# Optimization experiments

Measured on AMD Instinct MI355X. Metric: run time of the kernel, lower is better.

The kernel has to match this reference:

```python
import jax, jax.numpy as jnp
import numpy as np

D_MODEL = 4096
EXPERTS = 64
TOPK = 2


def setup_inputs() -> dict:
    key = jax.random.key(0)
    kx, kw = jax.random.split(key)
    x = jax.random.normal(kx, (4, 4096, D_MODEL), dtype=jnp.float32)
    # nn.Linear(input_size, expert_num, bias=False) weight, stored as [D, E] for x @ W
    W = jax.random.normal(kw, (D_MODEL, EXPERTS), dtype=jnp.float32) * (1.0 / np.sqrt(D_MODEL))
    return {"x": x, "W": W}


def reference(x, W):
    # logits = GateL(x): [B, S, E]
    logits = jnp.einsum("bsd,de->bse", x, W)
    y = jax.nn.softmax(logits, axis=-1)
    # top-k mask: scatter ones at top-k expert slots, zero elsewhere
    _, topk_idx = jax.lax.top_k(y, TOPK)            # [B, S, k]
    mask = jnp.sum(jax.nn.one_hot(topk_idx, EXPERTS, dtype=y.dtype), axis=-2)  # [B, S, E]
    y = y * mask
    return (y, logits)
```

## Files before the change

kernel.cpp:

```cpp
#include <hip/hip_runtime.h>
#include <hip/hip_bf16.h>


typedef float f32x4 __attribute__((ext_vector_type(4)));
typedef __bf16 bf16x8 __attribute__((ext_vector_type(8)));

#define MFMA16(a, b, c) __builtin_amdgcn_mfma_f32_16x16x32_bf16((a), (b), (c), 0, 0, 0)

__device__ __forceinline__ void gload_lds16(const void* g, void* l) {
  __builtin_amdgcn_global_load_lds((const __attribute__((address_space(1))) void*)g,
                                   (__attribute__((address_space(3))) void*)l, 16, 0, 0);
}

__global__ __launch_bounds__(256) void k_prep_w(const float* __restrict__ W,
                                                __bf16* __restrict__ wsW) {
  const int c = blockIdx.x;
  const int t = threadIdx.x;
  const int e = t & 63;
  const int q = t >> 6;
  const int nh = e >> 5, ntl = (e >> 4) & 1, ln = e & 15;
  bf16x8 hi8, lo8;
#pragma unroll
  for (int j = 0; j < 8; ++j) {
    const float w = W[(size_t)(c * 32 + q * 8 + j) * 64 + e];
    const __bf16 h = (__bf16)w;
    hi8[j] = h;
    lo8[j] = (__bf16)(w - (float)h);
  }
  __bf16* base = wsW + (size_t)c * 4096 + nh * 2048 + ntl * 1024 + q * 128 + ln * 8;
  *(bf16x8*)base = hi8;
  *(bf16x8*)(base + 512) = lo8;
}

__device__ __forceinline__ void split8(const f32x4 a, const f32x4 b,
                                       bf16x8& hi, bf16x8& lo) {
  const float f[8] = {a.x, a.y, a.z, a.w, b.x, b.y, b.z, b.w};
#pragma unroll
  for (int i = 0; i < 8; ++i) {
    const unsigned u = __builtin_bit_cast(unsigned, f[i]);
    hi[i] = __builtin_bit_cast(__bf16, (unsigned short)(u >> 16));
    lo[i] = (__bf16)(f[i] - __builtin_bit_cast(float, u & 0xFFFF0000u));
  }
}

__global__ __launch_bounds__(256, 2) void k_gate(const float* __restrict__ x,
                                                 const __bf16* __restrict__ wsW,
                                                 float* __restrict__ y,
                                                 float* __restrict__ logits) {
  __shared__ __align__(16) char smem[57344];
  const int t = threadIdx.x, w = t >> 6, l = t & 63;
  const int tb = blockIdx.x * 32;
  const int mt = w & 1, nh = w >> 1;
  const int q = l >> 4, ln = l & 15;

  char* xw = smem + w * 6144;
  char* ww = smem + 24576 + w * 8192;

  const int r0 = l >> 3, g0 = (l & 7) ^ (r0 & 7);
  const int r1 = 8 + (l >> 3), g1 = (l & 7) ^ (r1 & 7);
  const float* xp0 = x + (size_t)(tb + mt * 16 + r0) * 4096 + g0 * 4;
  const float* xp1 = x + (size_t)(tb + mt * 16 + r1) * 4096 + g1 * 4;
  const __bf16* wg = wsW + nh * 2048 + l * 8;

  const int rA = ln;
  const int offA0 = (rA * 8 + ((2 * q) ^ (rA & 7))) * 16;
  const int offA1 = (rA * 8 + ((2 * q + 1) ^ (rA & 7))) * 16;
  const int offW = q * 256 + ln * 16;

  auto stageX = [&](int st, int c) {
    char* d = xw + st * 2048 + l * 16;
    gload_lds16(xp0 + (size_t)c * 32, d);
    gload_lds16(xp1 + (size_t)c * 32, d + 1024);
  };
  auto stageW = [&](int st, int c) {
    char* d = ww + st * 4096 + l * 16;
    const __bf16* s = wg + (size_t)c * 4096;
    gload_lds16(s, d);
    gload_lds16(s + 512, d + 1024);
    gload_lds16(s + 1024, d + 2048);
    gload_lds16(s + 1536, d + 3072);
  };

  f32x4 acc0 = {0.f, 0.f, 0.f, 0.f};
  f32x4 acc1 = {0.f, 0.f, 0.f, 0.f};

  stageX(0, 0); stageW(0, 0); stageX(1, 1); stageW(1, 1); stageX(2, 2);

  int st = 0, stw = 0;
  for (int c = 0; c < 128; ++c) {
    if (c < 126)       asm volatile("s_waitcnt vmcnt(8)" ::: "memory");
    else if (c == 126) asm volatile("s_waitcnt vmcnt(6)" ::: "memory");
    else               asm volatile("s_waitcnt vmcnt(0)" ::: "memory");

    const char* xb = xw + st * 2048;
    const char* wb = ww + stw * 4096;
    const f32x4 A = *(const f32x4*)(xb + offA0);
    const f32x4 B = *(const f32x4*)(xb + offA1);
    const bf16x8 wh0 = *(const bf16x8*)(wb + offW);
    const bf16x8 wl0 = *(const bf16x8*)(wb + offW + 1024);
    const bf16x8 wh1 = *(const bf16x8*)(wb + offW + 2048);
    const bf16x8 wl1 = *(const bf16x8*)(wb + offW + 3072);

    bf16x8 ah, al;
    split8(A, B, ah, al);
    acc0 = MFMA16(ah, wh0, acc0);
    acc0 = MFMA16(al, wh0, acc0);
    acc0 = MFMA16(ah, wl0, acc0);
    acc0 = MFMA16(al, wl0, acc0);
    acc1 = MFMA16(ah, wh1, acc1);
    acc1 = MFMA16(al, wh1, acc1);
    acc1 = MFMA16(ah, wl1, acc1);
    acc1 = MFMA16(al, wl1, acc1);

    if (c < 126) stageW(stw, c + 2);
    if (c < 125) stageX(st, c + 3);
    st = (st == 2) ? 0 : st + 1;
    stw ^= 1;
  }

  __syncthreads();
  float* lt = (float*)smem;
  const int col = nh * 32 + ln;
#pragma unroll
  for (int r = 0; r < 4; ++r) {
    const int row = mt * 16 + q * 4 + r;
    lt[row * 65 + col] = acc0[r];
    lt[row * 65 + col + 16] = acc1[r];
    logits[(size_t)(tb + row) * 64 + col] = acc0[r];
    logits[(size_t)(tb + row) * 64 + col + 16] = acc1[r];
  }
  __syncthreads();

#pragma unroll
  for (int i = 0; i < 8; ++i) {
    const int tok = w * 8 + i;
    const float v = lt[tok * 65 + l];
    float bv = v; int bi = l;
    for (int off = 32; off; off >>= 1) {
      const float ov = __shfl_xor(bv, off);
      const int oi = __shfl_xor(bi, off);
      if (ov > bv || (ov == bv && oi < bi)) { bv = ov; bi = oi; }
    }
    const int i1 = bi;
    const float m1 = bv;
    float cv = (l == i1) ? -3.402823466e38f : v;
    int ci = l;
    for (int off = 32; off; off >>= 1) {
      const float ov = __shfl_xor(cv, off);
      const int oi = __shfl_xor(ci, off);
      if (ov > cv || (ov == cv && oi < ci)) { cv = ov; ci = oi; }
    }
    const float e = __expf(v - m1);
    float s = e;
    for (int off = 32; off; off >>= 1) s += __shfl_xor(s, off);
    y[(size_t)(tb + tok) * 64 + l] = (l == i1 || l == ci) ? (e / s) : 0.0f;
  }
}

extern "C" void kernel_launch(void* const* d_in, const int* in_sizes, int n_in,
                              void* d_out, int out_size, void* d_ws, size_t ws_size,
                              hipStream_t stream) {
  (void)in_sizes; (void)n_in; (void)out_size; (void)ws_size;
  const float* x = (const float*)d_in[0];
  const float* W = (const float*)d_in[1];
  float* out = (float*)d_out;
  float* yout = out;
  float* logits = out + 1048576;
  __bf16* wsW = (__bf16*)d_ws;

  k_prep_w<<<128, 256, 0, stream>>>(W, wsW);
  k_gate<<<512, 256, 0, stream>>>(x, wsW, yout, logits);
}
```

Before: 415.7 us.

## Shrink gate tile to 16 tokens with shared x buffer and register W prefetch

Each block now handles 16 tokens instead of 32, and the grid doubles to 1024 blocks. The four waves split the 64 experts between them and share one double-buffered LDS tile of x instead of each wave staging its own x and W. W fragments are prefetched directly into registers from global memory one chunk ahead, and a __syncthreads per iteration replaces the manual vmcnt pipeline. The goal is lower LDS use and higher occupancy (launch bounds 4 blocks per CU). The cost is a barrier every chunk, a shallower prefetch depth, and W being reloaded by twice as many blocks.

```diff
diff --git a/kernel.cpp b/kernel.cpp
--- a/kernel.cpp
+++ b/kernel.cpp
@@ -43,97 +43,66 @@
   }
 }
 
-__global__ __launch_bounds__(256, 2) void k_gate(const float* __restrict__ x,
+__global__ __launch_bounds__(256, 4) void k_gate(const float* __restrict__ x,
                                                  const __bf16* __restrict__ wsW,
                                                  float* __restrict__ y,
                                                  float* __restrict__ logits) {
-  __shared__ __align__(16) char smem[57344];
+  __shared__ __align__(16) char xs[2][2048];
+  __shared__ float lt[16 * 65];
+
   const int t = threadIdx.x, w = t >> 6, l = t & 63;
-  const int tb = blockIdx.x * 32;
-  const int mt = w & 1, nh = w >> 1;
+  const int tb = blockIdx.x * 16;
   const int q = l >> 4, ln = l & 15;
 
-  char* xw = smem + w * 6144;
-  char* ww = smem + 24576 + w * 8192;
+  const int sr = w * 8 + (l >> 3);
+  const int sg = (l & 7) ^ (sr & 7);
+  const float* xp = x + (size_t)(tb + sr) * 4096 + sg * 4;
 
-  const int r0 = l >> 3, g0 = (l & 7) ^ (r0 & 7);
-  const int r1 = 8 + (l >> 3), g1 = (l & 7) ^ (r1 & 7);
-  const float* xp0 = x + (size_t)(tb + mt * 16 + r0) * 4096 + g0 * 4;
-  const float* xp1 = x + (size_t)(tb + mt * 16 + r1) * 4096 + g1 * 4;
-  const __bf16* wg = wsW + nh * 2048 + l * 8;
+  const char* wgp = (const char*)wsW + (w >> 1) * 4096 + (w & 1) * 2048 + q * 256 + ln * 16;
 
-  const int rA = ln;
-  const int offA0 = (rA * 8 + ((2 * q) ^ (rA & 7))) * 16;
-  const int offA1 = (rA * 8 + ((2 * q + 1) ^ (rA & 7))) * 16;
-  const int offW = q * 256 + ln * 16;
+  const int offA0 = (ln * 8 + ((2 * q) ^ (ln & 7))) * 16;
+  const int offA1 = (ln * 8 + ((2 * q + 1) ^ (ln & 7))) * 16;
 
-  auto stageX = [&](int st, int c) {
-    char* d = xw + st * 2048 + l * 16;
-    gload_lds16(xp0 + (size_t)c * 32, d);
-    gload_lds16(xp1 + (size_t)c * 32, d + 1024);
-  };
-  auto stageW = [&](int st, int c) {
-    char* d = ww + st * 4096 + l * 16;
-    const __bf16* s = wg + (size_t)c * 4096;
-    gload_lds16(s, d);
-    gload_lds16(s + 512, d + 1024);
-    gload_lds16(s + 1024, d + 2048);
-    gload_lds16(s + 1536, d + 3072);
-  };
+  f32x4 acc = {0.f, 0.f, 0.f, 0.f};
 
-  f32x4 acc0 = {0.f, 0.f, 0.f, 0.f};
-  f32x4 acc1 = {0.f, 0.f, 0.f, 0.f};
+  if (w < 2) gload_lds16(xp, &xs[0][(w * 64 + l) * 16]);
+  bf16x8 whc = *(const bf16x8*)(wgp);
+  bf16x8 wlc = *(const bf16x8*)(wgp + 1024);
+  __syncthreads();
 
-  stageX(0, 0); stageW(0, 0); stageX(1, 1); stageW(1, 1); stageX(2, 2);
-
-  int st = 0, stw = 0;
   for (int c = 0; c < 128; ++c) {
-    if (c < 126)       asm volatile("s_waitcnt vmcnt(8)" ::: "memory");
-    else if (c == 126) asm volatile("s_waitcnt vmcnt(6)" ::: "memory");
-    else               asm volatile("s_waitcnt vmcnt(0)" ::: "memory");
-
-    const char* xb = xw + st * 2048;
-    const char* wb = ww + stw * 4096;
+    bf16x8 whn, wln;
+    if (c + 1 < 128) {
+      whn = *(const bf16x8*)(wgp + (size_t)(c + 1) * 8192);
+      wln = *(const bf16x8*)(wgp + (size_t)(c + 1) * 8192 + 1024);
+      if (w < 2) gload_lds16(xp + (size_t)(c + 1) * 32,
+                             &xs[(c + 1) & 1][(w * 64 + l) * 16]);
+    }
+    const char* xb = xs[c & 1];
     const f32x4 A = *(const f32x4*)(xb + offA0);
     const f32x4 B = *(const f32x4*)(xb + offA1);
-    const bf16x8 wh0 = *(const bf16x8*)(wb + offW);
-    const bf16x8 wl0 = *(const bf16x8*)(wb + offW + 1024);
-    const bf16x8 wh1 = *(const bf16x8*)(wb + offW + 2048);
-    const bf16x8 wl1 = *(const bf16x8*)(wb + offW + 3072);
-
     bf16x8 ah, al;
     split8(A, B, ah, al);
-    acc0 = MFMA16(ah, wh0, acc0);
-    acc0 = MFMA16(al, wh0, acc0);
-    acc0 = MFMA16(ah, wl0, acc0);
-    acc0 = MFMA16(al, wl0, acc0);
-    acc1 = MFMA16(ah, wh1, acc1);
-    acc1 = MFMA16(al, wh1, acc1);
-    acc1 = MFMA16(ah, wl1, acc1);
-    acc1 = MFMA16(al, wl1, acc1);
-
-    if (c < 126) stageW(stw, c + 2);
-    if (c < 125) stageX(st, c + 3);
-    st = (st == 2) ? 0 : st + 1;
-    stw ^= 1;
+    acc = MFMA16(ah, whc, acc);
+    acc = MFMA16(al, whc, acc);
+    acc = MFMA16(ah, wlc, acc);
+    acc = MFMA16(al, wlc, acc);
+    __syncthreads();
+    whc = whn; wlc = wln;
   }
 
-  __syncthreads();
-  float* lt = (float*)smem;
-  const int col = nh * 32 + ln;
+  const int col = w * 16 + ln;
 #pragma unroll
   for (int r = 0; r < 4; ++r) {
-    const int row = mt * 16 + q * 4 + r;
-    lt[row * 65 + col] = acc0[r];
-    lt[row * 65 + col + 16] = acc1[r];
-    logits[(size_t)(tb + row) * 64 + col] = acc0[r];
-    logits[(size_t)(tb + row) * 64 + col + 16] = acc1[r];
+    const int row = q * 4 + r;
+    lt[row * 65 + col] = acc[r];
+    logits[(size_t)(tb + row) * 64 + col] = acc[r];
   }
   __syncthreads();
 
 #pragma unroll
-  for (int i = 0; i < 8; ++i) {
-    const int tok = w * 8 + i;
+  for (int i = 0; i < 4; ++i) {
+    const int tok = w * 4 + i;
     const float v = lt[tok * 65 + l];
     float bv = v; int bi = l;
     for (int off = 32; off; off >>= 1) {
@@ -169,5 +138,5 @@
   __bf16* wsW = (__bf16*)d_ws;
 
   k_prep_w<<<128, 256, 0, stream>>>(W, wsW);
-  k_gate<<<512, 256, 0, stream>>>(x, wsW, yout, logits);
+  k_gate<<<1024, 256, 0, stream>>>(x, wsW, yout, logits);
 }
```

Result: faster. 401.9 us (-3.3%).
